# Performance work log

Hardware: AMD Instinct MI355X
Metric: run time of the kernel (lower is better)

Reference implementation:

```python
import jax, jax.numpy as jnp
import numpy as np

N = 50000      # nodes per object type (2 types)
F = 128        # input feature dim (num_feat)
H = 64         # FLAGS.hidden1 == FLAGS.hidden2
E = 800000     # edges per relation
NET = 4        # edge types: (0,0),(0,1),(1,0),(1,1); for k: dst type i=k//2, src type j=k%2


def setup_inputs() -> dict:
    key = jax.random.key(0)
    ks = jax.random.split(key, 7)
    x0 = jax.random.normal(ks[0], (N, F), jnp.float32)
    x1 = jax.random.normal(ks[1], (N, F), jnp.float32)
    src = jax.random.randint(ks[2], (NET, E), 0, N, jnp.int32)
    dst = jax.random.randint(ks[3], (NET, E), 0, N, jnp.int32)
    # normalized adjacency values (~1/avg_degree keeps activations stable)
    ew = jax.random.uniform(ks[4], (NET, E), jnp.float32) / 16.0
    W1 = jax.random.normal(ks[5], (NET, F, H), jnp.float32) / np.sqrt(F).astype(np.float32)
    Wl = jax.random.normal(ks[6], (NET, NET, H, H), jnp.float32) / np.sqrt(H).astype(np.float32)
    return {"x0": x0, "x1": x1, "src": src, "dst": dst, "ew": ew, "W1": W1, "Wl": Wl}


def _spmm(src_k, dst_k, w_k, x):
    # sparse [N_i, N_j] adjacency @ dense x: gather + weighted scatter-add
    return jax.ops.segment_sum(w_k[:, None] * x[src_k], dst_k, num_segments=N)


def _layer(xs, Ws, src, dst, ew, relu):
    # xs: [x_type0, x_type1]; per edge type (i,j): out[i] += A_ij @ (x_j @ W_ij)
    outs = [jnp.zeros((N, Ws.shape[-1]), xs[0].dtype) for _ in range(2)]
    for k in range(NET):
        i, j = k // 2, k % 2
        outs[i] = outs[i] + _spmm(src[k], dst[k], ew[k], xs[j] @ Ws[k])
    if relu:
        outs = [jax.nn.relu(o) for o in outs]
    return outs


def reference(x0, x1, src, dst, ew, W1, Wl):
    h1 = _layer([x0, x1], W1, src, dst, ew, relu=True)       # hidden1
    e1 = _layer(h1, Wl[0], src, dst, ew, relu=True)          # embeddings1
    e2 = _layer(e1, Wl[1], src, dst, ew, relu=True)          # embeddings2
    e3 = _layer(e2, Wl[2], src, dst, ew, relu=True)          # embeddings3
    emb = _layer(e3, Wl[3], src, dst, ew, relu=False)        # embeddings = add_n(reltyp4), no relu
    # final concat per object type: [hidden1, embeddings1, embeddings] -> (N, 3H)
    return jnp.stack([jnp.concatenate([h1[t], e1[t], emb[t]], axis=1) for t in range(2)])
```

## Files before the change

### kernel.cpp

```cpp
#include <hip/hip_runtime.h>
#include <cstddef>

#define NREL 4
#define NSUP 2
#define HD 64
#define FD 128
#define BSHIFT 8
#define BUCKET 256
#define CHUNK 16384

static inline int idiv_up(int a, int b) { return (a + b - 1) / b; }

typedef __attribute__((ext_vector_type(8))) short bf16x8;
typedef __attribute__((ext_vector_type(4))) float f32x4;

__device__ __forceinline__ unsigned short f2bf(float f) {
    unsigned int u = __float_as_uint(f);
    unsigned int r = (u + 0x7FFFu + ((u >> 16) & 1u)) >> 16;
    return (unsigned short)r;
}
__device__ __forceinline__ float bflo(unsigned int v) {
    return __uint_as_float(v << 16);
}
__device__ __forceinline__ float bfhi(unsigned int v) {
    return __uint_as_float(v & 0xFFFF0000u);
}


__global__ void bhist_kernel(const int* __restrict__ dst, int* __restrict__ bhist,
                             int E2, int NBP) {
    int k = blockIdx.y;
    extern __shared__ int lh[];
    for (int i = threadIdx.x; i < NBP; i += blockDim.x) lh[i] = 0;
    __syncthreads();
    const int* dk = dst + (size_t)k * E2;
    for (int e = blockIdx.x * blockDim.x + threadIdx.x; e < E2; e += gridDim.x * blockDim.x)
        atomicAdd(&lh[dk[e] >> BSHIFT], 1);
    __syncthreads();
    int* bh = bhist + (size_t)k * NBP;
    for (int i = threadIdx.x; i < NBP; i += blockDim.x)
        if (lh[i]) atomicAdd(&bh[i], lh[i]);
}


__global__ void bscan_kernel(const int* __restrict__ bhist, int* __restrict__ bptr,
                             int* __restrict__ gcur, int NBP, int E2) {
    int k = blockIdx.x;
    __shared__ int wsum[16];
    int tid = threadIdx.x, wid = tid >> 6, lane = tid & 63;
    int v = (tid < NBP) ? bhist[(size_t)k * NBP + tid] : 0;
    int x = v;
    #pragma unroll
    for (int off = 1; off < 64; off <<= 1) {
        int y = __shfl_up(x, off, 64);
        if (lane >= off) x += y;
    }
    if (lane == 63) wsum[wid] = x;
    __syncthreads();
    if (wid == 0) {
        int s = (lane < 16) ? wsum[lane] : 0;
        #pragma unroll
        for (int off = 1; off < 16; off <<= 1) {
            int y = __shfl_up(s, off, 64);
            if (lane >= off) s += y;
        }
        if (lane < 16) wsum[lane] = s;
    }
    __syncthreads();
    int excl = x - v + (wid ? wsum[wid - 1] : 0);
    if (tid < NBP) {
        bptr[(size_t)k * (NBP + 1) + tid] = excl;
        gcur[(size_t)k * NBP + tid] = excl;
    }
    if (tid == 0) bptr[(size_t)k * (NBP + 1) + NBP] = E2;
}


__global__ void part_kernel(const int* __restrict__ src, const int* __restrict__ dst,
                            const float* __restrict__ ew, int* __restrict__ gcur,
                            int2* __restrict__ staged, int E, int E2, int N, int NBP) {
    int k = blockIdx.y;
    extern __shared__ int sh[];
    int* lcnt = sh;
    int* lbase = sh + NBP;
    for (int i = threadIdx.x; i < NBP; i += blockDim.x) lcnt[i] = 0;
    __syncthreads();
    const int* sk = src + (size_t)k * E2;
    const int* dk = dst + (size_t)k * E2;
    const float* wk = ew + (size_t)k * E2;
    int base = blockIdx.x * CHUNK;
    int n = min(CHUNK, E2 - base);
    for (int i = threadIdx.x; i < n; i += blockDim.x)
        atomicAdd(&lcnt[dk[base + i] >> BSHIFT], 1);
    __syncthreads();
    for (int i = threadIdx.x; i < NBP; i += blockDim.x) {
        int c = lcnt[i];
        lbase[i] = c ? atomicAdd(&gcur[(size_t)k * NBP + i], c) : 0;
    }
    __syncthreads();
    for (int i = threadIdx.x; i < NBP; i += blockDim.x) lcnt[i] = 0;
    __syncthreads();
    int2* out = staged + (size_t)k * E2;
    for (int i = threadIdx.x; i < n; i += blockDim.x) {
        int gi = base + i;
        int d = dk[gi];
        int b = d >> BSHIFT;
        int row = sk[gi] + ((gi >= E) ? N : 0);
        int local = atomicAdd(&lcnt[b], 1);
        out[lbase[b] + local] =
            make_int2(row | ((d & (BUCKET - 1)) << 17), __float_as_int(wk[gi]));
    }
}


__global__ void bsort_kernel(const int2* __restrict__ staged, const int* __restrict__ bptr,
                             int* __restrict__ rowptr, unsigned int* __restrict__ edges,
                             int E2, int N, int NBP) {
    int k = blockIdx.y;
    int b = blockIdx.x;
    __shared__ int hist[BUCKET];
    __shared__ int excl[BUCKET];
    __shared__ int cur[BUCKET];
    __shared__ int wsum2[4];
    int tid = threadIdx.x;
    int wid = tid >> 6, lane = tid & 63;
    if (tid < BUCKET) hist[tid] = 0;
    __syncthreads();
    int beg = bptr[(size_t)k * (NBP + 1) + b];
    int end = bptr[(size_t)k * (NBP + 1) + b + 1];
    const int2* in = staged + (size_t)k * E2;
    for (int i = beg + tid; i < end; i += blockDim.x)
        atomicAdd(&hist[(in[i].x >> 17) & (BUCKET - 1)], 1);
    __syncthreads();
    int v = 0, x = 0;
    if (tid < BUCKET) {
        v = hist[tid];
        x = v;
        #pragma unroll
        for (int off = 1; off < 64; off <<= 1) {
            int y = __shfl_up(x, off, 64);
            if (lane >= off) x += y;
        }
        if (lane == 63) wsum2[wid] = x;
    }
    __syncthreads();
    if (tid == 0) {
        int s = 0;
        #pragma unroll
        for (int j = 0; j < 4; ++j) { int t = wsum2[j]; wsum2[j] = s; s += t; }
    }
    __syncthreads();
    if (tid < BUCKET) {
        int e = x - v + wsum2[wid];
        excl[tid] = e;
        cur[tid] = e;
    }
    __syncthreads();
    unsigned int* outp = edges + (size_t)k * E2;
    for (int i = beg + tid; i < end; i += blockDim.x) {
        int2 q = in[i];
        int dl = (q.x >> 17) & (BUCKET - 1);
        int pos = atomicAdd(&cur[dl], 1);
        unsigned int wb = (unsigned int)(f2bf(__int_as_float(q.y)) & 0x7FFF);
        outp[beg + pos] = ((unsigned int)q.x & 0x1FFFFu) | (wb << 17);
    }
    int node0 = b * BUCKET;
    if (tid < BUCKET && node0 + tid < N)
        rowptr[(size_t)k * (N + 1) + node0 + tid] = beg + excl[tid];
    if (b == 0 && tid == 0) rowptr[(size_t)k * (N + 1) + N] = E2;
}


__global__ void convx_kernel(const float* __restrict__ x0, const float* __restrict__ x1,
                             unsigned short* __restrict__ xb, int nq ) {
    for (int i = blockIdx.x * blockDim.x + threadIdx.x; i < 2 * nq;
         i += gridDim.x * blockDim.x) {
        const float4* xs = (i < nq) ? (const float4*)x0 : (const float4*)x1;
        int j = (i < nq) ? i : i - nq;
        float4 v = xs[j];
        ushort4 o;
        o.x = f2bf(v.x); o.y = f2bf(v.y); o.z = f2bf(v.z); o.w = f2bf(v.w);
        reinterpret_cast<ushort4*>(xb)[i] = o;
    }
}

__global__ void convw_kernel(const float* __restrict__ W, unsigned short* __restrict__ Wf,
                             int mats, int KK) {
    int tid = blockIdx.x * blockDim.x + threadIdx.x;
    int total = mats * KK * 4 * 64;
    if (tid >= total) return;
    int l = tid & 63;
    int n = (tid >> 6) & 3;
    int rest = tid >> 8;
    int kk = rest % KK;
    int mat = rest / KK;
    int h = l >> 4, c = l & 15;
    int K = KK * 32;
    const float* Wm = W + (size_t)mat * K * 64;
    unsigned short* o = Wf + (size_t)tid * 8;
    #pragma unroll
    for (int i = 0; i < 8; ++i)
        o[i] = f2bf(Wm[(size_t)(kk * 32 + h * 8 + i) * 64 + n * 16 + c]);
}


template <int K>
__global__ void gemm_mfma_kernel(const unsigned short* __restrict__ Xb,
                                 const unsigned short* __restrict__ Wf,
                                 unsigned short* __restrict__ Ybase, int N) {
    constexpr int KK = K / 32;
    int rel = blockIdx.y;
    const unsigned short* X = Xb + (size_t)(rel & 1) * N * K;
    const bf16x8* Wv = reinterpret_cast<const bf16x8*>(Wf + (size_t)rel * KK * 4 * 64 * 8);
    unsigned short* Y = Ybase + (size_t)rel * N * HD;
    int tid = threadIdx.x;
    int w = tid >> 6, l = tid & 63;
    int lr = l & 15, lh = l >> 4;
    int row0 = blockIdx.x * 128 + w * 32;
    f32x4 acc00 = {0.f,0.f,0.f,0.f}, acc01 = {0.f,0.f,0.f,0.f};
    f32x4 acc02 = {0.f,0.f,0.f,0.f}, acc03 = {0.f,0.f,0.f,0.f};
    f32x4 acc10 = {0.f,0.f,0.f,0.f}, acc11 = {0.f,0.f,0.f,0.f};
    f32x4 acc12 = {0.f,0.f,0.f,0.f}, acc13 = {0.f,0.f,0.f,0.f};
    int r0 = min(row0 + lr, N - 1);
    int r1 = min(row0 + 16 + lr, N - 1);
    const unsigned short* xp0 = X + (size_t)r0 * K + lh * 8;
    const unsigned short* xp1 = X + (size_t)r1 * K + lh * 8;
    #pragma unroll
    for (int kk = 0; kk < KK; ++kk) {
        bf16x8 a0 = *reinterpret_cast<const bf16x8*>(xp0 + kk * 32);
        bf16x8 a1 = *reinterpret_cast<const bf16x8*>(xp1 + kk * 32);
        bf16x8 b0 = Wv[(kk * 4 + 0) * 64 + l];
        bf16x8 b1 = Wv[(kk * 4 + 1) * 64 + l];
        bf16x8 b2 = Wv[(kk * 4 + 2) * 64 + l];
        bf16x8 b3 = Wv[(kk * 4 + 3) * 64 + l];
        acc00 = __builtin_amdgcn_mfma_f32_16x16x32_bf16(a0, b0, acc00, 0, 0, 0);
        acc01 = __builtin_amdgcn_mfma_f32_16x16x32_bf16(a0, b1, acc01, 0, 0, 0);
        acc02 = __builtin_amdgcn_mfma_f32_16x16x32_bf16(a0, b2, acc02, 0, 0, 0);
        acc03 = __builtin_amdgcn_mfma_f32_16x16x32_bf16(a0, b3, acc03, 0, 0, 0);
        acc10 = __builtin_amdgcn_mfma_f32_16x16x32_bf16(a1, b0, acc10, 0, 0, 0);
        acc11 = __builtin_amdgcn_mfma_f32_16x16x32_bf16(a1, b1, acc11, 0, 0, 0);
        acc12 = __builtin_amdgcn_mfma_f32_16x16x32_bf16(a1, b2, acc12, 0, 0, 0);
        acc13 = __builtin_amdgcn_mfma_f32_16x16x32_bf16(a1, b3, acc13, 0, 0, 0);
    }
    #pragma unroll
    for (int reg = 0; reg < 4; ++reg) {
        int rowa = row0 + lh * 4 + reg;
        if (rowa < N) {
            unsigned short* yp = Y + (size_t)rowa * HD + lr;
            yp[0]  = f2bf(acc00[reg]);
            yp[16] = f2bf(acc01[reg]);
            yp[32] = f2bf(acc02[reg]);
            yp[48] = f2bf(acc03[reg]);
        }
        int rowb = row0 + 16 + lh * 4 + reg;
        if (rowb < N) {
            unsigned short* yp = Y + (size_t)rowb * HD + lr;
            yp[0]  = f2bf(acc10[reg]);
            yp[16] = f2bf(acc11[reg]);
            yp[32] = f2bf(acc12[reg]);
            yp[48] = f2bf(acc13[reg]);
        }
    }
}


__global__ void spmm_kernel(const unsigned short* __restrict__ Ybase,
                            const int* __restrict__ rowptr, const unsigned int* __restrict__ edges,
                            unsigned short* __restrict__ act, float* __restrict__ outp,
                            int N, int E2, int relu) {
    int id = blockIdx.x;
    int g = id & 7;
    int t = g >> 2;
    int pbi = (id >> 3) * 4 + (g & 3);
    int wave = threadIdx.x >> 6;
    int lane = threadIdx.x & 63;
    int d = pbi * 4 + wave;
    if (d >= N) return;
    int h = lane >> 4;
    int c4 = (lane & 15) * 4;
    const unsigned short* Y = Ybase + (size_t)(2 * t) * N * HD;
    const unsigned int* ep = edges + (size_t)t * E2;
    int beg = rowptr[(size_t)t * (N + 1) + d];
    int end = rowptr[(size_t)t * (N + 1) + d + 1];
    float4 a0 = {0.f,0.f,0.f,0.f}, a1 = {0.f,0.f,0.f,0.f};
    float4 a2 = {0.f,0.f,0.f,0.f}, a3 = {0.f,0.f,0.f,0.f};
    if (beg < end) {
        int endm1 = end - 1;
        unsigned int m0, m1, m2, m3;
        {
            int i0 = beg + 0 + h, i1 = beg + 4 + h, i2 = beg + 8 + h, i3 = beg + 12 + h;
            m0 = ep[i0 < end ? i0 : endm1];
            m1 = ep[i1 < end ? i1 : endm1];
            m2 = ep[i2 < end ? i2 : endm1];
            m3 = ep[i3 < end ? i3 : endm1];
        }
        for (int base = beg; ; ) {
            int nb = base + 16;
            bool more = nb < end;
            unsigned int n0, n1, n2, n3;
            if (more) {
                int i0 = nb + 0 + h, i1 = nb + 4 + h, i2 = nb + 8 + h, i3 = nb + 12 + h;
                n0 = ep[i0 < end ? i0 : endm1];
                n1 = ep[i1 < end ? i1 : endm1];
                n2 = ep[i2 < end ? i2 : endm1];
                n3 = ep[i3 < end ? i3 : endm1];
            }
            uint2 y0 = *reinterpret_cast<const uint2*>(Y + ((m0 & 0x1FFFFu) * HD + c4));
            uint2 y1 = *reinterpret_cast<const uint2*>(Y + ((m1 & 0x1FFFFu) * HD + c4));
            uint2 y2 = *reinterpret_cast<const uint2*>(Y + ((m2 & 0x1FFFFu) * HD + c4));
            uint2 y3 = *reinterpret_cast<const uint2*>(Y + ((m3 & 0x1FFFFu) * HD + c4));
            float w0 = ((base + 0 + h) < end) ? __uint_as_float((m0 >> 17) << 16) : 0.f;
            float w1 = ((base + 4 + h) < end) ? __uint_as_float((m1 >> 17) << 16) : 0.f;
            float w2 = ((base + 8 + h) < end) ? __uint_as_float((m2 >> 17) << 16) : 0.f;
            float w3 = ((base + 12 + h) < end) ? __uint_as_float((m3 >> 17) << 16) : 0.f;
            a0.x += w0 * bflo(y0.x); a0.y += w0 * bfhi(y0.x);
            a0.z += w0 * bflo(y0.y); a0.w += w0 * bfhi(y0.y);
            a1.x += w1 * bflo(y1.x); a1.y += w1 * bfhi(y1.x);
            a1.z += w1 * bflo(y1.y); a1.w += w1 * bfhi(y1.y);
            a2.x += w2 * bflo(y2.x); a2.y += w2 * bfhi(y2.x);
            a2.z += w2 * bflo(y2.y); a2.w += w2 * bfhi(y2.y);
            a3.x += w3 * bflo(y3.x); a3.y += w3 * bfhi(y3.x);
            a3.z += w3 * bflo(y3.y); a3.w += w3 * bfhi(y3.y);
            if (!more) break;
            base = nb;
            m0 = n0; m1 = n1; m2 = n2; m3 = n3;
        }
    }
    float4 s;
    s.x = (a0.x + a1.x) + (a2.x + a3.x);
    s.y = (a0.y + a1.y) + (a2.y + a3.y);
    s.z = (a0.z + a1.z) + (a2.z + a3.z);
    s.w = (a0.w + a1.w) + (a2.w + a3.w);
    s.x += __shfl_xor(s.x, 16, 64);  s.x += __shfl_xor(s.x, 32, 64);
    s.y += __shfl_xor(s.y, 16, 64);  s.y += __shfl_xor(s.y, 32, 64);
    s.z += __shfl_xor(s.z, 16, 64);  s.z += __shfl_xor(s.z, 32, 64);
    s.w += __shfl_xor(s.w, 16, 64);  s.w += __shfl_xor(s.w, 32, 64);
    if (relu) {
        s.x = fmaxf(s.x, 0.f); s.y = fmaxf(s.y, 0.f);
        s.z = fmaxf(s.z, 0.f); s.w = fmaxf(s.w, 0.f);
    }
    if (lane < 16) {
        if (act) {
            ushort4 ob;
            ob.x = f2bf(s.x); ob.y = f2bf(s.y); ob.z = f2bf(s.z); ob.w = f2bf(s.w);
            *reinterpret_cast<ushort4*>(&act[((size_t)t * N + d) * HD + c4]) = ob;
        }
        if (outp) *reinterpret_cast<float4*>(&outp[((size_t)t * N + d) * 192 + c4]) = s;
    }
}


extern "C" void kernel_launch(void* const* d_in, const int* in_sizes, int n_in,
                              void* d_out, int out_size, void* d_ws, size_t ws_size,
                              hipStream_t stream) {
    const float* x0 = (const float*)d_in[0];
    const float* x1 = (const float*)d_in[1];
    const int* src = (const int*)d_in[2];
    const int* dst = (const int*)d_in[3];
    const float* ew = (const float*)d_in[4];
    const float* W1 = (const float*)d_in[5];
    const float* Wl = (const float*)d_in[6];
    float* out = (float*)d_out;

    int N = in_sizes[0] / FD;
    int E = in_sizes[2] / NREL;
    int E2 = 2 * E;
    int NBP = idiv_up(N, BUCKET);

    char* ws = (char*)d_ws;
    size_t off = 0;
    auto alloc = [&](size_t bytes) -> void* {
        void* p = ws + off;
        off = (off + bytes + 255) & ~(size_t)255;
        return p;
    };
    int* bhist   = (int*)alloc((size_t)NSUP * NBP * 4);
    int* bptr    = (int*)alloc((size_t)NSUP * (NBP + 1) * 4);
    int* gcur    = (int*)alloc((size_t)NSUP * NBP * 4);
    int* rowptr  = (int*)alloc((size_t)NSUP * (N + 1) * 4);
    unsigned int* edges = (unsigned int*)alloc((size_t)NSUP * E2 * 4);
    unsigned short* y    = (unsigned short*)alloc((size_t)NREL * N * HD * 2);
    unsigned short* xb   = (unsigned short*)alloc((size_t)2 * N * FD * 2);
    unsigned short* actb = (unsigned short*)alloc((size_t)2 * N * HD * 2);
    unsigned short* W1f  = (unsigned short*)alloc((size_t)NREL * 4 * 4 * 64 * 8 * 2);
    unsigned short* Wlf  = (unsigned short*)alloc((size_t)16 * 2 * 4 * 64 * 8 * 2);
    int2* staged = (int2*)alloc((size_t)NSUP * E2 * 8);
    (void)ws_size;

    int nq = N * FD / 4;
    convx_kernel<<<2048, 256, 0, stream>>>(x0, x1, xb, nq);
    convw_kernel<<<idiv_up(NREL * 4 * 4 * 64, 256), 256, 0, stream>>>(W1, W1f, NREL, 4);
    convw_kernel<<<idiv_up(16 * 2 * 4 * 64, 256), 256, 0, stream>>>(Wl, Wlf, 16, 2);

    hipMemsetAsync(bhist, 0, (size_t)NSUP * NBP * 4, stream);
    bhist_kernel<<<dim3(384, NSUP), 256, NBP * 4, stream>>>(dst, bhist, E2, NBP);
    bscan_kernel<<<NSUP, 1024, 0, stream>>>(bhist, bptr, gcur, NBP, E2);
    part_kernel<<<dim3(idiv_up(E2, CHUNK), NSUP), 1024, 2 * NBP * 4, stream>>>(
        src, dst, ew, gcur, staged, E, E2, N, NBP);
    bsort_kernel<<<dim3(NBP, NSUP), 1024, 0, stream>>>(staged, bptr, rowptr, edges, E2, N, NBP);

    dim3 ggrid(idiv_up(N, 128), NREL);
    int NB4 = idiv_up(N, 4);
    int sgx = idiv_up(NB4, 4) * 8;

    gemm_mfma_kernel<FD><<<ggrid, 256, 0, stream>>>(xb, W1f, y, N);
    spmm_kernel<<<sgx, 256, 0, stream>>>(y, rowptr, edges, actb, out + 0, N, E2, 1);

    for (int l = 0; l < 4; ++l) {
        gemm_mfma_kernel<HD><<<ggrid, 256, 0, stream>>>(
            actb, Wlf + (size_t)l * 4 * 2 * 4 * 64 * 8, y, N);
        float* op = (l == 0) ? (out + 64) : (l == 3) ? (out + 128) : nullptr;
        unsigned short* ap = (l == 3) ? nullptr : actb;
        int relu = (l == 3) ? 0 : 1;
        spmm_kernel<<<sgx, 256, 0, stream>>>(y, rowptr, edges, ap, op, N, E2, relu);
    }
}
```

Baseline: 432.6 us.

## Fuse input bf16 conversion into first GEMM and deepen SpMM gather unroll

The separate kernel converting fp32 node features to bf16 is removed; the first-layer MFMA GEMM now reads fp32 rows directly and packs them to bf16 with a hardware pack-convert instruction. This drops a full read/write pass over the inputs and one launch, but the GEMM now loads twice as many bytes per row. The SpMM gather loop is also widened from 16 to 32 edges per iteration, issuing 8 independent row loads per lane to raise memory-level parallelism at the cost of more registers.

New measurement: 451.0 us. +4.3%, slower.

```diff
diff --git a/kernel.cpp b/kernel.cpp
--- a/kernel.cpp
+++ b/kernel.cpp
@@ -24,6 +24,11 @@
 }
 __device__ __forceinline__ float bfhi(unsigned int v) {
     return __uint_as_float(v & 0xFFFF0000u);
+}
+__device__ __forceinline__ unsigned int cvtpk_bf16(float lo, float hi) {
+    unsigned int r;
+    asm("v_cvt_pk_bf16_f32 %0, %1, %2" : "=v"(r) : "v"(lo), "v"(hi));
+    return r;
 }
 
 
@@ -170,19 +175,6 @@
     if (b == 0 && tid == 0) rowptr[(size_t)k * (N + 1) + N] = E2;
 }
 
-
-__global__ void convx_kernel(const float* __restrict__ x0, const float* __restrict__ x1,
-                             unsigned short* __restrict__ xb, int nq ) {
-    for (int i = blockIdx.x * blockDim.x + threadIdx.x; i < 2 * nq;
-         i += gridDim.x * blockDim.x) {
-        const float4* xs = (i < nq) ? (const float4*)x0 : (const float4*)x1;
-        int j = (i < nq) ? i : i - nq;
-        float4 v = xs[j];
-        ushort4 o;
-        o.x = f2bf(v.x); o.y = f2bf(v.y); o.z = f2bf(v.z); o.w = f2bf(v.w);
-        reinterpret_cast<ushort4*>(xb)[i] = o;
-    }
-}
 
 __global__ void convw_kernel(const float* __restrict__ W, unsigned short* __restrict__ Wf,
                              int mats, int KK) {
@@ -264,6 +256,80 @@
 }
 
 
+__global__ void gemm_mfma_f32in_kernel(const float* __restrict__ X0,
+                                       const float* __restrict__ X1,
+                                       const unsigned short* __restrict__ Wf,
+                                       unsigned short* __restrict__ Ybase, int N) {
+    constexpr int K = FD;
+    constexpr int KK = K / 32;
+    int rel = blockIdx.y;
+    const float* X = (rel & 1) ? X1 : X0;
+    const bf16x8* Wv = reinterpret_cast<const bf16x8*>(Wf + (size_t)rel * KK * 4 * 64 * 8);
+    unsigned short* Y = Ybase + (size_t)rel * N * HD;
+    int tid = threadIdx.x;
+    int w = tid >> 6, l = tid & 63;
+    int lr = l & 15, lh = l >> 4;
+    int row0 = blockIdx.x * 128 + w * 32;
+    f32x4 acc00 = {0.f,0.f,0.f,0.f}, acc01 = {0.f,0.f,0.f,0.f};
+    f32x4 acc02 = {0.f,0.f,0.f,0.f}, acc03 = {0.f,0.f,0.f,0.f};
+    f32x4 acc10 = {0.f,0.f,0.f,0.f}, acc11 = {0.f,0.f,0.f,0.f};
+    f32x4 acc12 = {0.f,0.f,0.f,0.f}, acc13 = {0.f,0.f,0.f,0.f};
+    int r0 = min(row0 + lr, N - 1);
+    int r1 = min(row0 + 16 + lr, N - 1);
+    const float* xp0 = X + (size_t)r0 * K + lh * 8;
+    const float* xp1 = X + (size_t)r1 * K + lh * 8;
+    #pragma unroll
+    for (int kk = 0; kk < KK; ++kk) {
+        float4 xa0 = *reinterpret_cast<const float4*>(xp0 + kk * 32);
+        float4 xa1 = *reinterpret_cast<const float4*>(xp0 + kk * 32 + 4);
+        float4 xb0 = *reinterpret_cast<const float4*>(xp1 + kk * 32);
+        float4 xb1 = *reinterpret_cast<const float4*>(xp1 + kk * 32 + 4);
+        union { unsigned int u[4]; bf16x8 v; } ca, cb;
+        ca.u[0] = cvtpk_bf16(xa0.x, xa0.y);
+        ca.u[1] = cvtpk_bf16(xa0.z, xa0.w);
+        ca.u[2] = cvtpk_bf16(xa1.x, xa1.y);
+        ca.u[3] = cvtpk_bf16(xa1.z, xa1.w);
+        cb.u[0] = cvtpk_bf16(xb0.x, xb0.y);
+        cb.u[1] = cvtpk_bf16(xb0.z, xb0.w);
+        cb.u[2] = cvtpk_bf16(xb1.x, xb1.y);
+        cb.u[3] = cvtpk_bf16(xb1.z, xb1.w);
+        bf16x8 a0 = ca.v;
+        bf16x8 a1 = cb.v;
+        bf16x8 b0 = Wv[(kk * 4 + 0) * 64 + l];
+        bf16x8 b1 = Wv[(kk * 4 + 1) * 64 + l];
+        bf16x8 b2 = Wv[(kk * 4 + 2) * 64 + l];
+        bf16x8 b3 = Wv[(kk * 4 + 3) * 64 + l];
+        acc00 = __builtin_amdgcn_mfma_f32_16x16x32_bf16(a0, b0, acc00, 0, 0, 0);
+        acc01 = __builtin_amdgcn_mfma_f32_16x16x32_bf16(a0, b1, acc01, 0, 0, 0);
+        acc02 = __builtin_amdgcn_mfma_f32_16x16x32_bf16(a0, b2, acc02, 0, 0, 0);
+        acc03 = __builtin_amdgcn_mfma_f32_16x16x32_bf16(a0, b3, acc03, 0, 0, 0);
+        acc10 = __builtin_amdgcn_mfma_f32_16x16x32_bf16(a1, b0, acc10, 0, 0, 0);
+        acc11 = __builtin_amdgcn_mfma_f32_16x16x32_bf16(a1, b1, acc11, 0, 0, 0);
+        acc12 = __builtin_amdgcn_mfma_f32_16x16x32_bf16(a1, b2, acc12, 0, 0, 0);
+        acc13 = __builtin_amdgcn_mfma_f32_16x16x32_bf16(a1, b3, acc13, 0, 0, 0);
+    }
+    #pragma unroll
+    for (int reg = 0; reg < 4; ++reg) {
+        int rowa = row0 + lh * 4 + reg;
+        if (rowa < N) {
+            unsigned short* yp = Y + (size_t)rowa * HD + lr;
+            yp[0]  = f2bf(acc00[reg]);
+            yp[16] = f2bf(acc01[reg]);
+            yp[32] = f2bf(acc02[reg]);
+            yp[48] = f2bf(acc03[reg]);
+        }
+        int rowb = row0 + 16 + lh * 4 + reg;
+        if (rowb < N) {
+            unsigned short* yp = Y + (size_t)rowb * HD + lr;
+            yp[0]  = f2bf(acc10[reg]);
+            yp[16] = f2bf(acc11[reg]);
+            yp[32] = f2bf(acc12[reg]);
+            yp[48] = f2bf(acc13[reg]);
+        }
+    }
+}
+
+
 __global__ void spmm_kernel(const unsigned short* __restrict__ Ybase,
                             const int* __restrict__ rowptr, const unsigned int* __restrict__ edges,
                             unsigned short* __restrict__ act, float* __restrict__ outp,
@@ -282,55 +348,52 @@
     const unsigned int* ep = edges + (size_t)t * E2;
     int beg = rowptr[(size_t)t * (N + 1) + d];
     int end = rowptr[(size_t)t * (N + 1) + d + 1];
-    float4 a0 = {0.f,0.f,0.f,0.f}, a1 = {0.f,0.f,0.f,0.f};
-    float4 a2 = {0.f,0.f,0.f,0.f}, a3 = {0.f,0.f,0.f,0.f};
+    float4 a[4];
+    #pragma unroll
+    for (int j = 0; j < 4; ++j) a[j] = make_float4(0.f, 0.f, 0.f, 0.f);
     if (beg < end) {
         int endm1 = end - 1;
-        unsigned int m0, m1, m2, m3;
-        {
-            int i0 = beg + 0 + h, i1 = beg + 4 + h, i2 = beg + 8 + h, i3 = beg + 12 + h;
-            m0 = ep[i0 < end ? i0 : endm1];
-            m1 = ep[i1 < end ? i1 : endm1];
-            m2 = ep[i2 < end ? i2 : endm1];
-            m3 = ep[i3 < end ? i3 : endm1];
+        unsigned int m[8];
+        #pragma unroll
+        for (int j = 0; j < 8; ++j) {
+            int idx = beg + 4 * j + h;
+            m[j] = ep[idx < end ? idx : endm1];
         }
         for (int base = beg; ; ) {
-            int nb = base + 16;
+            int nb = base + 32;
             bool more = nb < end;
-            unsigned int n0, n1, n2, n3;
+            unsigned int n[8];
             if (more) {
-                int i0 = nb + 0 + h, i1 = nb + 4 + h, i2 = nb + 8 + h, i3 = nb + 12 + h;
-                n0 = ep[i0 < end ? i0 : endm1];
-                n1 = ep[i1 < end ? i1 : endm1];
-                n2 = ep[i2 < end ? i2 : endm1];
-                n3 = ep[i3 < end ? i3 : endm1];
+                #pragma unroll
+                for (int j = 0; j < 8; ++j) {
+                    int idx = nb + 4 * j + h;
+                    n[j] = ep[idx < end ? idx : endm1];
+                }
             }
-            uint2 y0 = *reinterpret_cast<const uint2*>(Y + ((m0 & 0x1FFFFu) * HD + c4));
-            uint2 y1 = *reinterpret_cast<const uint2*>(Y + ((m1 & 0x1FFFFu) * HD + c4));
-            uint2 y2 = *reinterpret_cast<const uint2*>(Y + ((m2 & 0x1FFFFu) * HD + c4));
-            uint2 y3 = *reinterpret_cast<const uint2*>(Y + ((m3 & 0x1FFFFu) * HD + c4));
-            float w0 = ((base + 0 + h) < end) ? __uint_as_float((m0 >> 17) << 16) : 0.f;
-            float w1 = ((base + 4 + h) < end) ? __uint_as_float((m1 >> 17) << 16) : 0.f;
-            float w2 = ((base + 8 + h) < end) ? __uint_as_float((m2 >> 17) << 16) : 0.f;
-            float w3 = ((base + 12 + h) < end) ? __uint_as_float((m3 >> 17) << 16) : 0.f;
-            a0.x += w0 * bflo(y0.x); a0.y += w0 * bfhi(y0.x);
-            a0.z += w0 * bflo(y0.y); a0.w += w0 * bfhi(y0.y);
-            a1.x += w1 * bflo(y1.x); a1.y += w1 * bfhi(y1.x);
-            a1.z += w1 * bflo(y1.y); a1.w += w1 * bfhi(y1.y);
-            a2.x += w2 * bflo(y2.x); a2.y += w2 * bfhi(y2.x);
-            a2.z += w2 * bflo(y2.y); a2.w += w2 * bfhi(y2.y);
-            a3.x += w3 * bflo(y3.x); a3.y += w3 * bfhi(y3.x);
-            a3.z += w3 * bflo(y3.y); a3.w += w3 * bfhi(y3.y);
+            uint2 y[8];
+            #pragma unroll
+            for (int j = 0; j < 8; ++j)
+                y[j] = *reinterpret_cast<const uint2*>(Y + ((m[j] & 0x1FFFFu) * HD + c4));
+            #pragma unroll
+            for (int j = 0; j < 8; ++j) {
+                float w = ((base + 4 * j + h) < end)
+                              ? __uint_as_float((m[j] >> 17) << 16) : 0.f;
+                a[j & 3].x += w * bflo(y[j].x);
+                a[j & 3].y += w * bfhi(y[j].x);
+                a[j & 3].z += w * bflo(y[j].y);
+                a[j & 3].w += w * bfhi(y[j].y);
+            }
             if (!more) break;
             base = nb;
-            m0 = n0; m1 = n1; m2 = n2; m3 = n3;
+            #pragma unroll
+            for (int j = 0; j < 8; ++j) m[j] = n[j];
         }
     }
     float4 s;
-    s.x = (a0.x + a1.x) + (a2.x + a3.x);
-    s.y = (a0.y + a1.y) + (a2.y + a3.y);
-    s.z = (a0.z + a1.z) + (a2.z + a3.z);
-    s.w = (a0.w + a1.w) + (a2.w + a3.w);
+    s.x = (a[0].x + a[1].x) + (a[2].x + a[3].x);
+    s.y = (a[0].y + a[1].y) + (a[2].y + a[3].y);
+    s.z = (a[0].z + a[1].z) + (a[2].z + a[3].z);
+    s.w = (a[0].w + a[1].w) + (a[2].w + a[3].w);
     s.x += __shfl_xor(s.x, 16, 64);  s.x += __shfl_xor(s.x, 32, 64);
     s.y += __shfl_xor(s.y, 16, 64);  s.y += __shfl_xor(s.y, 32, 64);
     s.z += __shfl_xor(s.z, 16, 64);  s.z += __shfl_xor(s.z, 32, 64);
@@ -380,15 +443,12 @@
     int* rowptr  = (int*)alloc((size_t)NSUP * (N + 1) * 4);
     unsigned int* edges = (unsigned int*)alloc((size_t)NSUP * E2 * 4);
     unsigned short* y    = (unsigned short*)alloc((size_t)NREL * N * HD * 2);
-    unsigned short* xb   = (unsigned short*)alloc((size_t)2 * N * FD * 2);
     unsigned short* actb = (unsigned short*)alloc((size_t)2 * N * HD * 2);
     unsigned short* W1f  = (unsigned short*)alloc((size_t)NREL * 4 * 4 * 64 * 8 * 2);
     unsigned short* Wlf  = (unsigned short*)alloc((size_t)16 * 2 * 4 * 64 * 8 * 2);
     int2* staged = (int2*)alloc((size_t)NSUP * E2 * 8);
     (void)ws_size;
 
-    int nq = N * FD / 4;
-    convx_kernel<<<2048, 256, 0, stream>>>(x0, x1, xb, nq);
     convw_kernel<<<idiv_up(NREL * 4 * 4 * 64, 256), 256, 0, stream>>>(W1, W1f, NREL, 4);
     convw_kernel<<<idiv_up(16 * 2 * 4 * 64, 256), 256, 0, stream>>>(Wl, Wlf, 16, 2);
 
@@ -403,7 +463,7 @@
     int NB4 = idiv_up(N, 4);
     int sgx = idiv_up(NB4, 4) * 8;
 
-    gemm_mfma_kernel<FD><<<ggrid, 256, 0, stream>>>(xb, W1f, y, N);
+    gemm_mfma_f32in_kernel<<<ggrid, 256, 0, stream>>>(x0, x1, W1f, y, N);
     spmm_kernel<<<sgx, 256, 0, stream>>>(y, rowptr, edges, actb, out + 0, N, E2, 1);
 
     for (int l = 0; l < 4; ++l) {
```
